# Kernel optimization log

Hardware: AMD Instinct MI355X
Metric: run time of the kernel (lower is better)

## Reference

```python
import jax, jax.numpy as jnp
import numpy as np

N = 50000      # nodes
E = 800000     # edges (avg degree 16)
IN = 128       # in_feats
HID = 32       # hidden_feats per head
H = 4          # num_heads
NEG_SLOPE = 0.2


def setup_inputs() -> dict:
    key = jax.random.key(0)
    ks = jax.random.split(key, 13)
    x = jax.random.normal(ks[0], (N, IN), jnp.float32)
    src = jax.random.randint(ks[1], (E,), 0, N, jnp.int32)
    dst = jax.random.randint(ks[2], (E,), 0, N, jnp.int32)

    def lin(k, fi, fo):
        return jax.random.normal(k, (fi, fo), jnp.float32) * (1.0 / np.sqrt(fi))

    # conv1: IN -> H*HID
    W1 = lin(ks[3], IN, H * HID)
    al1 = jax.random.normal(ks[4], (H, HID), jnp.float32) * 0.1
    ar1 = jax.random.normal(ks[5], (H, HID), jnp.float32) * 0.1
    b1 = jnp.zeros((H, HID), jnp.float32)
    # conv2: H*HID -> H*HID
    W2 = lin(ks[6], H * HID, H * HID)
    al2 = jax.random.normal(ks[7], (H, HID), jnp.float32) * 0.1
    ar2 = jax.random.normal(ks[8], (H, HID), jnp.float32) * 0.1
    b2 = jnp.zeros((H, HID), jnp.float32)
    # fc: HID -> 1
    fcW = lin(ks[9], HID, 1)
    fcb = jnp.zeros((1,), jnp.float32)
    return {"x": x, "src": src, "dst": dst,
            "W1": W1, "al1": al1, "ar1": ar1, "b1": b1,
            "W2": W2, "al2": al2, "ar2": ar2, "b2": b2,
            "fcW": fcW, "fcb": fcb}


def gat_conv(x, src, dst, W, al, ar, b):
    # x: [N, F_in] -> feat: [N, H, HID]
    feat = (x @ W).reshape(N, H, HID)
    el = jnp.sum(feat * al, axis=-1)            # [N, H]
    er = jnp.sum(feat * ar, axis=-1)            # [N, H]
    e = jax.nn.leaky_relu(el[src] + er[dst], NEG_SLOPE)  # [E, H]
    # segment softmax over incoming edges of each dst node
    m = jax.ops.segment_max(e, dst, num_segments=N)      # [N, H]
    ex = jnp.exp(e - m[dst])                              # [E, H]
    denom = jax.ops.segment_sum(ex, dst, num_segments=N)  # [N, H]
    alpha = ex / denom[dst]                                # [E, H]
    msg = feat[src] * alpha[:, :, None]                    # [E, H, HID]
    out = jax.ops.segment_sum(msg, dst, num_segments=N)   # [N, H, HID]
    return out + b[None, :, :]


def reference(x, src, dst, W1, al1, ar1, b1, W2, al2, ar2, b2, fcW, fcb):
    h = gat_conv(x, src, dst, W1, al1, ar1, b1).reshape(N, H * HID)
    h = jax.nn.relu(h)
    # dropout(0.5) is identity in eval mode
    h = gat_conv(h, src, dst, W2, al2, ar2, b2).mean(axis=1)  # [N, HID]
    return h @ fcW + fcb                                       # [N, 1]
```

## Files before the change

### kernel.cpp

```cpp
#include <hip/hip_runtime.h>
#include <hip/hip_fp16.h>

#define LEAK 0.2f
#define CAP 64

static __device__ inline unsigned pack_h2(float a, float b) {
    __half2 h = __floats2half2_rn(a, b);
    unsigned u; __builtin_memcpy(&u, &h, 4); return u;
}
static __device__ inline float2 unpack_h2(unsigned u) {
    __half2 h; __builtin_memcpy(&h, &u, 4); return __half22float2(h);
}

__global__ __launch_bounds__(256) void k0(
    int* __restrict__ cnt, const float* __restrict__ W2,
    const float* __restrict__ al2, const float* __restrict__ ar2,
    const float* __restrict__ fcW, const float* __restrict__ b2,
    float* __restrict__ WfT, float* __restrict__ bc, int N, int zb) {
    const int t = threadIdx.x;
    int i = blockIdx.x * 256 + t;
    if (i < N) cnt[i] = 0;
    int fb = blockIdx.x - zb;
    if (fb >= 0) {
        int idx = fb * 256 + t;
        if (idx < 1536) {
            int c = idx >> 7, k = idx & 127;
            int h = c & 3, sel = c >> 2;
            const float* vec = (sel == 0) ? (al2 + 32 * h)
                             : (sel == 1) ? (ar2 + 32 * h) : fcW;
            float s = 0.f;
#pragma unroll 8
            for (int m = 0; m < 32; m++) s += W2[k * 128 + 32 * h + m] * vec[m];
            WfT[c * 128 + k] = s;
        } else if (idx < 1540) {
            int h = idx - 1536;
            float s = 0.f;
            for (int m = 0; m < 32; m++) s += b2[h * 32 + m] * fcW[m];
            bc[h] = s;
        }
    }
}

__global__ __launch_bounds__(256, 4) void k1(
    const float* __restrict__ X, const float* __restrict__ W,
    const float* __restrict__ al, const float* __restrict__ ar,
    float* __restrict__ elh, float* __restrict__ erh,
    uint2* __restrict__ fh2,
    const int* __restrict__ src, const int* __restrict__ dst,
    int* __restrict__ cnt, int* __restrict__ ell,
    int N, int E, int ntiles) {
    __shared__ float sW[32 * 128];
    __shared__ float sXT[32 * 128];
    const int b = blockIdx.x;
    const int t = threadIdx.x;

    if (b < ntiles) {
        const int r0 = b * 128;
        const int tx = t & 15;
        const int ty = t >> 4;
        const float4* X4 = (const float4*)X;
        const float4* W4 = (const float4*)W;
        float4* sW4 = (float4*)sW;
        const float4* sXT4 = (const float4*)sXT;

        float4 acc[8][2];
#pragma unroll
        for (int r = 0; r < 8; r++) {
            acc[r][0] = make_float4(0.f, 0.f, 0.f, 0.f);
            acc[r][1] = make_float4(0.f, 0.f, 0.f, 0.f);
        }
        for (int ks = 0; ks < 4; ++ks) {
            if (ks) __syncthreads();
#pragma unroll
            for (int i = 0; i < 4; i++) {
                int idx = i * 256 + t;
                sW4[idx] = W4[1024 * ks + idx];
            }
#pragma unroll
            for (int i = 0; i < 4; i++) {
                int idx = i * 256 + t;
                int row = idx >> 3;
                int kq = idx & 7;
                float4 v = make_float4(0.f, 0.f, 0.f, 0.f);
                if (r0 + row < N) v = X4[(size_t)(r0 + row) * 32 + ks * 8 + kq];
                int sc = (((row >> 2) ^ kq)) * 4 + (row & 3);
                sXT[(4 * kq + 0) * 128 + sc] = v.x;
                sXT[(4 * kq + 1) * 128 + sc] = v.y;
                sXT[(4 * kq + 2) * 128 + sc] = v.z;
                sXT[(4 * kq + 3) * 128 + sc] = v.w;
            }
            __syncthreads();
#pragma unroll 4
            for (int k = 0; k < 32; k++) {
                float4 w0 = sW4[k * 32 + tx];
                float4 w1 = sW4[k * 32 + 16 + tx];
                float4 x0 = sXT4[k * 32 + (ty ^ (k >> 2))];
                float4 x1 = sXT4[k * 32 + ((16 + ty) ^ (k >> 2))];
                float xs[8] = {x0.x, x0.y, x0.z, x0.w, x1.x, x1.y, x1.z, x1.w};
#pragma unroll
                for (int r = 0; r < 8; r++) {
                    acc[r][0].x += xs[r] * w0.x; acc[r][0].y += xs[r] * w0.y;
                    acc[r][0].z += xs[r] * w0.z; acc[r][0].w += xs[r] * w0.w;
                    acc[r][1].x += xs[r] * w1.x; acc[r][1].y += xs[r] * w1.y;
                    acc[r][1].z += xs[r] * w1.z; acc[r][1].w += xs[r] * w1.w;
                }
            }
        }
        const float4* al4p = (const float4*)al;
        const float4* ar4p = (const float4*)ar;
        float4 alA = al4p[tx], alB = al4p[16 + tx];
        float4 arA = ar4p[tx], arB = ar4p[16 + tx];
        const int hA = tx >> 3;
        const int hB = 2 + (tx >> 3);
        const int pA = tx & 7;
#pragma unroll
        for (int r = 0; r < 8; r++) {
            int lrow = (r < 4) ? (ty * 4 + r) : (64 + ty * 4 + (r - 4));
            int row = r0 + lrow;
            bool ok = row < N;
            float4 a0 = acc[r][0], a1 = acc[r][1];
            if (ok) {
                uint2 d0, d1;
                d0.x = pack_h2(a0.x, a0.y); d0.y = pack_h2(a0.z, a0.w);
                d1.x = pack_h2(a1.x, a1.y); d1.y = pack_h2(a1.z, a1.w);
                fh2[((size_t)hA * N + row) * 8 + pA] = d0;
                fh2[((size_t)hB * N + row) * 8 + pA] = d1;
            }
            float elA = a0.x * alA.x + a0.y * alA.y + a0.z * alA.z + a0.w * alA.w;
            float erA = a0.x * arA.x + a0.y * arA.y + a0.z * arA.z + a0.w * arA.w;
            float elB = a1.x * alB.x + a1.y * alB.y + a1.z * alB.z + a1.w * alB.w;
            float erB = a1.x * arB.x + a1.y * arB.y + a1.z * arB.z + a1.w * arB.w;
#pragma unroll
            for (int off = 1; off < 8; off <<= 1) {
                elA += __shfl_xor(elA, off); erA += __shfl_xor(erA, off);
                elB += __shfl_xor(elB, off); erB += __shfl_xor(erB, off);
            }
            if (ok && tx == 0) {
                elh[(size_t)0 * N + row] = elA; erh[(size_t)0 * N + row] = erA;
                elh[(size_t)2 * N + row] = elB; erh[(size_t)2 * N + row] = erB;
            }
            if (ok && tx == 8) {
                elh[(size_t)1 * N + row] = elA; erh[(size_t)1 * N + row] = erA;
                elh[(size_t)3 * N + row] = elB; erh[(size_t)3 * N + row] = erB;
            }
        }
    } else {
        const int nbe = gridDim.x - ntiles;
        for (int e = (b - ntiles) * 256 + t; e < E; e += nbe * 256) {
            int s = src[e], d = dst[e];
            int pos = atomicAdd(&cnt[d], 1);
            if (pos < CAP) ell[(size_t)d * CAP + pos] = s;
        }
    }
}

__global__ __launch_bounds__(256) void k_agg1(
    const uint2* __restrict__ fh2, const float* __restrict__ elh,
    const float* __restrict__ erh, const int* __restrict__ ell,
    const int* __restrict__ cnt, const float* __restrict__ b1,
    uint2* __restrict__ h1h2, int N, int ngrp) {
    const int wave = threadIdx.x >> 6;
    const int lane = threadIdx.x & 63;
    const int b = blockIdx.x;
    const int h = (b & 7) >> 1;
    const int g = (b >> 3) * 2 + (b & 1);
    if (g >= ngrp) return;
    const int nsub = lane >> 3;
    const int p = lane & 7;
    const int n = g * 32 + wave * 8 + nsub;
    const bool nok = n < N;

    int deg = 0;
    float er = 0.f;
    if (nok) {
        deg = cnt[n]; if (deg > CAP) deg = CAP;
        er = erh[(size_t)h * N + n];
    }
    const float* elp = elh + (size_t)h * N;
    const uint2* fhp = fh2 + (size_t)h * N * 8;
    const int* row = ell + (size_t)(nok ? n : 0) * CAP;

    float a0 = 0.f, a1 = 0.f, a2 = 0.f, a3 = 0.f, den = 0.f;
    int j = 0;
    for (; j + 3 < deg; j += 4) {
        int s0 = row[j], s1 = row[j + 1], s2 = row[j + 2], s3 = row[j + 3];
        float e0 = elp[s0] + er;
        float e1 = elp[s1] + er;
        float e2 = elp[s2] + er;
        float e3 = elp[s3] + er;
        uint2 u0 = fhp[(size_t)s0 * 8 + p];
        uint2 u1 = fhp[(size_t)s1 * 8 + p];
        uint2 u2 = fhp[(size_t)s2 * 8 + p];
        uint2 u3 = fhp[(size_t)s3 * 8 + p];
        e0 = fmaxf(e0, LEAK * e0); float w0 = __expf(e0);
        e1 = fmaxf(e1, LEAK * e1); float w1 = __expf(e1);
        e2 = fmaxf(e2, LEAK * e2); float w2 = __expf(e2);
        e3 = fmaxf(e3, LEAK * e3); float w3 = __expf(e3);
        float2 f00 = unpack_h2(u0.x), f01 = unpack_h2(u0.y);
        float2 f10 = unpack_h2(u1.x), f11 = unpack_h2(u1.y);
        float2 f20 = unpack_h2(u2.x), f21 = unpack_h2(u2.y);
        float2 f30 = unpack_h2(u3.x), f31 = unpack_h2(u3.y);
        a0 += w0 * f00.x + w1 * f10.x + w2 * f20.x + w3 * f30.x;
        a1 += w0 * f00.y + w1 * f10.y + w2 * f20.y + w3 * f30.y;
        a2 += w0 * f01.x + w1 * f11.x + w2 * f21.x + w3 * f31.x;
        a3 += w0 * f01.y + w1 * f11.y + w2 * f21.y + w3 * f31.y;
        den += (w0 + w1) + (w2 + w3);
    }
    for (; j < deg; ++j) {
        int s = row[j];
        float e = elp[s] + er;
        uint2 u = fhp[(size_t)s * 8 + p];
        e = fmaxf(e, LEAK * e); float w = __expf(e);
        float2 f0 = unpack_h2(u.x), f1 = unpack_h2(u.y);
        a0 += w * f0.x; a1 += w * f0.y; a2 += w * f1.x; a3 += w * f1.y;
        den += w;
    }
    float inv = (den > 0.f) ? (1.0f / den) : 0.f;
    float4 bb = ((const float4*)b1)[h * 8 + p];
    a0 = fmaxf(a0 * inv + bb.x, 0.f);
    a1 = fmaxf(a1 * inv + bb.y, 0.f);
    a2 = fmaxf(a2 * inv + bb.z, 0.f);
    a3 = fmaxf(a3 * inv + bb.w, 0.f);
    if (nok) {
        uint2 d; d.x = pack_h2(a0, a1); d.y = pack_h2(a2, a3);
        h1h2[(size_t)n * 32 + h * 8 + p] = d;
    }
}

__global__ __launch_bounds__(256) void k_P(const uint2* __restrict__ h1h2,
                                           const float* __restrict__ WfT_g,
                                           float2* __restrict__ Pag,
                                           float* __restrict__ er2, int n_nodes) {
    __shared__ float sW[12 * 128];
    for (int i = threadIdx.x; i < 1536; i += 256) sW[i] = WfT_g[i];
    __syncthreads();
    int g = threadIdx.x >> 4;
    int q = threadIdx.x & 15;
    int n = blockIdx.x * 16 + g;
    if (n >= n_nodes) return;
    uint4 raw = ((const uint4*)h1h2)[(size_t)n * 16 + q];
    float2 f0 = unpack_h2(raw.x), f1 = unpack_h2(raw.y);
    float2 f2 = unpack_h2(raw.z), f3 = unpack_h2(raw.w);
    float hv[8] = {f0.x, f0.y, f1.x, f1.y, f2.x, f2.y, f3.x, f3.y};
    float p[12];
#pragma unroll
    for (int c = 0; c < 12; c++) {
        const float* wr = &sW[c * 128 + q * 8];
        float4 wa = *(const float4*)wr;
        float4 wb = *(const float4*)(wr + 4);
        p[c] = hv[0] * wa.x + hv[1] * wa.y + hv[2] * wa.z + hv[3] * wa.w
             + hv[4] * wb.x + hv[5] * wb.y + hv[6] * wb.z + hv[7] * wb.w;
    }
#pragma unroll
    for (int off = 1; off < 16; off <<= 1) {
#pragma unroll
        for (int c = 0; c < 12; c++) p[c] += __shfl_xor(p[c], off);
    }
    if (q < 4) Pag[(size_t)n * 4 + q] = make_float2(p[q], p[8 + q]);
    else if (q < 8) er2[(size_t)n * 4 + (q - 4)] = p[q];
}

__global__ __launch_bounds__(256) void k_agg2(const float2* __restrict__ Pag,
                                              const float* __restrict__ er2,
                                              const int* __restrict__ ell,
                                              const int* __restrict__ cnt,
                                              const float* __restrict__ bc,
                                              const float* __restrict__ fcb,
                                              float* __restrict__ out, int N) {
    int idx = blockIdx.x * 256 + threadIdx.x;
    int n = idx >> 2, h = idx & 3;
    if (n >= N) return;
    int deg = cnt[n]; if (deg > CAP) deg = CAP;
    float er = er2[(size_t)n * 4 + h];
    const int* row = ell + (size_t)n * CAP;
    float num = 0.f, den = 0.f;
    int j = 0, d4 = deg & ~3;
    for (; j < d4; j += 4) {
        int s0 = row[j], s1 = row[j + 1], s2 = row[j + 2], s3 = row[j + 3];
        float2 g0 = Pag[(size_t)s0 * 4 + h];
        float2 g1 = Pag[(size_t)s1 * 4 + h];
        float2 g2 = Pag[(size_t)s2 * 4 + h];
        float2 g3 = Pag[(size_t)s3 * 4 + h];
        float e0 = g0.x + er; e0 = fmaxf(e0, LEAK * e0); float w0 = __expf(e0);
        float e1 = g1.x + er; e1 = fmaxf(e1, LEAK * e1); float w1 = __expf(e1);
        float e2 = g2.x + er; e2 = fmaxf(e2, LEAK * e2); float w2 = __expf(e2);
        float e3 = g3.x + er; e3 = fmaxf(e3, LEAK * e3); float w3 = __expf(e3);
        num += w0 * g0.y + w1 * g1.y + w2 * g2.y + w3 * g3.y;
        den += (w0 + w1) + (w2 + w3);
    }
    for (; j < deg; ++j) {
        int s = row[j];
        float2 gg = Pag[(size_t)s * 4 + h];
        float e = gg.x + er; e = fmaxf(e, LEAK * e);
        float w = __expf(e);
        num += w * gg.y; den += w;
    }
    float r = (den > 0.f) ? (num / den) : 0.f;
    r += bc[h];
    r += __shfl_xor(r, 1);
    r += __shfl_xor(r, 2);
    if (h == 0) out[n] = 0.25f * r + fcb[0];
}

extern "C" void kernel_launch(void* const* d_in, const int* in_sizes, int n_in,
                              void* d_out, int out_size, void* d_ws, size_t ws_size,
                              hipStream_t stream) {
    const float* x   = (const float*)d_in[0];
    const int* src   = (const int*)d_in[1];
    const int* dst   = (const int*)d_in[2];
    const float* W1  = (const float*)d_in[3];
    const float* al1 = (const float*)d_in[4];
    const float* ar1 = (const float*)d_in[5];
    const float* b1  = (const float*)d_in[6];
    const float* W2  = (const float*)d_in[7];
    const float* al2 = (const float*)d_in[8];
    const float* ar2 = (const float*)d_in[9];
    const float* b2  = (const float*)d_in[10];
    const float* fcW = (const float*)d_in[11];
    const float* fcb = (const float*)d_in[12];
    float* out = (float*)d_out;

    const int N = in_sizes[0] / 128;
    const int E = in_sizes[1];

    char* w = (char*)d_ws;
    size_t off = 0;
    auto alloc = [&](size_t bytes) {
        void* p = w + off;
        off = (off + bytes + 255) & ~(size_t)255;
        return p;
    };
    uint2* fh2   = (uint2*)alloc((size_t)4 * N * 8 * 8);
    uint2* h1h2  = (uint2*)alloc((size_t)N * 32 * 8);
    float* elh   = (float*)alloc((size_t)4 * N * 4);
    float* erhp  = (float*)alloc((size_t)4 * N * 4);
    float2* Pag  = (float2*)alloc((size_t)N * 4 * 8);
    float* er2   = (float*)alloc((size_t)N * 4 * 4);
    float* WfT   = (float*)alloc((size_t)(12 * 128 + 4) * 4);
    float* bc    = WfT + 12 * 128;
    int* cnt     = (int*)alloc((size_t)N * 4);
    int* ell     = (int*)alloc((size_t)N * CAP * 4);

    const int zb = (N + 255) / 256;
    const int ntiles = (N + 127) / 128;
    const int ellB = (E + 1023) / 1024;
    const int ngrp = (N + 31) / 32;
    const int agg1_blocks = ((ngrp + 1) / 2) * 8;

    k0<<<zb + 8, 256, 0, stream>>>(cnt, W2, al2, ar2, fcW, b2, WfT, bc, N, zb);
    k1<<<ntiles + ellB, 256, 0, stream>>>(x, W1, al1, ar1, elh, erhp, fh2,
                                          src, dst, cnt, ell, N, E, ntiles);
    k_agg1<<<agg1_blocks, 256, 0, stream>>>(fh2, elh, erhp, ell, cnt, b1, h1h2, N, ngrp);
    k_P<<<(N + 15) / 16, 256, 0, stream>>>(h1h2, WfT, Pag, er2, N);
    k_agg2<<<(N * 4 + 255) / 256, 256, 0, stream>>>(Pag, er2, ell, cnt, bc, fcb, out, N);
}
```

Measured before the change: 233.0 us.

## Store ELL neighbor indices as 16-bit and partition ELL build by destination range

Neighbor indices in the ELL adjacency are stored as unsigned short instead of int, and the aggregation kernels read four at a time with a ushort4 load. This halves the memory traffic for the adjacency. The ELL build now has each block scan a slice of edges but handle only one of eight destination-node ranges, which is meant to localize atomics and scattered writes. The cost is that every block reads dst for its whole slice. Node ids go up to N=50000, which fits in 16 bits, but anything above 65535 would be silently truncated.

```diff
diff --git a/kernel.cpp b/kernel.cpp
--- a/kernel.cpp
+++ b/kernel.cpp
@@ -47,8 +47,8 @@
     float* __restrict__ elh, float* __restrict__ erh,
     uint2* __restrict__ fh2,
     const int* __restrict__ src, const int* __restrict__ dst,
-    int* __restrict__ cnt, int* __restrict__ ell,
-    int N, int E, int ntiles) {
+    int* __restrict__ cnt, unsigned short* __restrict__ ell,
+    int N, int E, int ntiles, int nranks) {
     __shared__ float sW[32 * 128];
     __shared__ float sXT[32 * 128];
     const int b = blockIdx.x;
@@ -145,18 +145,29 @@
             }
         }
     } else {
-        const int nbe = gridDim.x - ntiles;
-        for (int e = (b - ntiles) * 256 + t; e < E; e += nbe * 256) {
-            int s = src[e], d = dst[e];
-            int pos = atomicAdd(&cnt[d], 1);
-            if (pos < CAP) ell[(size_t)d * CAP + pos] = s;
+        const int bE = b - ntiles;
+        const int part = bE & 7;
+        const int rank = bE >> 3;
+        const int S = (N + 7) >> 3;
+        const int lo = part * S;
+        const int hi = (lo + S < N) ? (lo + S) : N;
+        const int per = (E + nranks - 1) / nranks;
+        const int e0 = rank * per;
+        const int e1 = (e0 + per < E) ? (e0 + per) : E;
+        for (int e = e0 + t; e < e1; e += 256) {
+            int d = dst[e];
+            if (d >= lo && d < hi) {
+                int s = src[e];
+                int pos = atomicAdd(&cnt[d], 1);
+                if (pos < CAP) ell[(size_t)d * CAP + pos] = (unsigned short)s;
+            }
         }
     }
 }
 
 __global__ __launch_bounds__(256) void k_agg1(
     const uint2* __restrict__ fh2, const float* __restrict__ elh,
-    const float* __restrict__ erh, const int* __restrict__ ell,
+    const float* __restrict__ erh, const unsigned short* __restrict__ ell,
     const int* __restrict__ cnt, const float* __restrict__ b1,
     uint2* __restrict__ h1h2, int N, int ngrp) {
     const int wave = threadIdx.x >> 6;
@@ -178,12 +189,13 @@
     }
     const float* elp = elh + (size_t)h * N;
     const uint2* fhp = fh2 + (size_t)h * N * 8;
-    const int* row = ell + (size_t)(nok ? n : 0) * CAP;
+    const unsigned short* row = ell + (size_t)(nok ? n : 0) * CAP;
 
     float a0 = 0.f, a1 = 0.f, a2 = 0.f, a3 = 0.f, den = 0.f;
     int j = 0;
     for (; j + 3 < deg; j += 4) {
-        int s0 = row[j], s1 = row[j + 1], s2 = row[j + 2], s3 = row[j + 3];
+        ushort4 ss = *(const ushort4*)(row + j);
+        int s0 = ss.x, s1 = ss.y, s2 = ss.z, s3 = ss.w;
         float e0 = elp[s0] + er;
         float e1 = elp[s1] + er;
         float e2 = elp[s2] + er;
@@ -262,7 +274,7 @@
 
 __global__ __launch_bounds__(256) void k_agg2(const float2* __restrict__ Pag,
                                               const float* __restrict__ er2,
-                                              const int* __restrict__ ell,
+                                              const unsigned short* __restrict__ ell,
                                               const int* __restrict__ cnt,
                                               const float* __restrict__ bc,
                                               const float* __restrict__ fcb,
@@ -272,11 +284,12 @@
     if (n >= N) return;
     int deg = cnt[n]; if (deg > CAP) deg = CAP;
     float er = er2[(size_t)n * 4 + h];
-    const int* row = ell + (size_t)n * CAP;
+    const unsigned short* row = ell + (size_t)n * CAP;
     float num = 0.f, den = 0.f;
     int j = 0, d4 = deg & ~3;
     for (; j < d4; j += 4) {
-        int s0 = row[j], s1 = row[j + 1], s2 = row[j + 2], s3 = row[j + 3];
+        ushort4 ss = *(const ushort4*)(row + j);
+        int s0 = ss.x, s1 = ss.y, s2 = ss.z, s3 = ss.w;
         float2 g0 = Pag[(size_t)s0 * 4 + h];
         float2 g1 = Pag[(size_t)s1 * 4 + h];
         float2 g2 = Pag[(size_t)s2 * 4 + h];
@@ -339,17 +352,18 @@
     float* WfT   = (float*)alloc((size_t)(12 * 128 + 4) * 4);
     float* bc    = WfT + 12 * 128;
     int* cnt     = (int*)alloc((size_t)N * 4);
-    int* ell     = (int*)alloc((size_t)N * CAP * 4);
+    unsigned short* ell = (unsigned short*)alloc((size_t)N * CAP * 2);
 
     const int zb = (N + 255) / 256;
     const int ntiles = (N + 127) / 128;
-    const int ellB = (E + 1023) / 1024;
+    const int nranks = 96;
+    const int ellB = nranks * 8;
     const int ngrp = (N + 31) / 32;
     const int agg1_blocks = ((ngrp + 1) / 2) * 8;
 
     k0<<<zb + 8, 256, 0, stream>>>(cnt, W2, al2, ar2, fcW, b2, WfT, bc, N, zb);
     k1<<<ntiles + ellB, 256, 0, stream>>>(x, W1, al1, ar1, elh, erhp, fh2,
-                                          src, dst, cnt, ell, N, E, ntiles);
+                                          src, dst, cnt, ell, N, E, ntiles, nranks);
     k_agg1<<<agg1_blocks, 256, 0, stream>>>(fh2, elh, erhp, ell, cnt, b1, h1h2, N, ngrp);
     k_P<<<(N + 15) / 16, 256, 0, stream>>>(h1h2, WfT, Pag, er2, N);
     k_agg2<<<(N * 4 + 255) / 256, 256, 0, stream>>>(Pag, er2, ell, cnt, bc, fcb, out, N);
```

After: 229.8 us. Within noise of the previous version (-1.4%).
